# Performance work log

Hardware: AMD Instinct MI355X
Metric: run time of the kernel (lower is better)

Reference implementation:

```python
import jax, jax.numpy as jnp
import numpy as np

N_NODES = 100000
N_EDGES = 1600000
D_IN = 64
D_HID = 64
D_OUT = 10
N_GRAPHS = 512


def setup_inputs() -> dict:
    key = jax.random.key(0)
    ks = jax.random.split(key, 12)
    x = jax.random.normal(ks[0], (N_NODES, D_IN), dtype=jnp.float32)
    edge_index = jax.random.randint(ks[1], (2, N_EDGES), 0, N_NODES, dtype=jnp.int64)
    batch = jnp.sort(jax.random.randint(ks[2], (N_NODES,), 0, N_GRAPHS, dtype=jnp.int64))
    def lin_w(k, fan_in, fan_out):
        s = 1.0 / np.sqrt(fan_in)
        return jax.random.uniform(k, (fan_in, fan_out), jnp.float32, -s, s)
    # Per PyG GraphConv: lin_rel (with bias) on aggregated neighbors, lin_root (no bias) on self.
    params = {
        'W_rel1': lin_w(ks[3], D_IN, D_HID),  'b_rel1': jnp.zeros((D_HID,), jnp.float32), 'W_root1': lin_w(ks[4], D_IN, D_HID),
        'W_rel2': lin_w(ks[5], D_HID, D_HID), 'b_rel2': jnp.zeros((D_HID,), jnp.float32), 'W_root2': lin_w(ks[6], D_HID, D_HID),
        'W_rel3': lin_w(ks[7], D_HID, D_HID), 'b_rel3': jnp.zeros((D_HID,), jnp.float32), 'W_root3': lin_w(ks[8], D_HID, D_HID),
        'W_lin': lin_w(ks[9], D_HID, D_OUT),  'b_lin': jnp.zeros((D_OUT,), jnp.float32),
    }
    return {'x': x, 'edge_index': edge_index, 'batch': batch, **params}


def _graph_conv(x, src, dst, W_rel, b_rel, W_root):
    # sum-aggregate messages x[src] at dst nodes, then two linear maps
    agg = jax.ops.segment_sum(x[src], dst, num_segments=N_NODES)
    return agg @ W_rel + b_rel + x @ W_root


def reference(x, edge_index, batch,
              W_rel1, b_rel1, W_root1,
              W_rel2, b_rel2, W_root2,
              W_rel3, b_rel3, W_root3,
              W_lin, b_lin):
    src, dst = edge_index[0], edge_index[1]
    h = jax.nn.relu(_graph_conv(x, src, dst, W_rel1, b_rel1, W_root1))
    h = jax.nn.relu(_graph_conv(h, src, dst, W_rel2, b_rel2, W_root2))
    h = _graph_conv(h, src, dst, W_rel3, b_rel3, W_root3)
    # global_mean_pool over graph ids
    sums = jax.ops.segment_sum(h, batch, num_segments=N_GRAPHS)
    counts = jax.ops.segment_sum(jnp.ones((h.shape[0], 1), h.dtype), batch, num_segments=N_GRAPHS)
    pooled = sums / jnp.maximum(counts, 1.0)
    return pooled @ W_lin + b_lin
```

## Files before the change

kernel.cpp:

```cpp
#include <hip/hip_runtime.h>

#define NN 100000
#define NE 1600000
#define DF 64
#define NG 512
#define DOUT 10
#define NPART 8
#define PSZ 12500

typedef unsigned short u16;
typedef unsigned int   u32;
typedef __attribute__((ext_vector_type(8))) short short8;
typedef __attribute__((ext_vector_type(4))) float f32x4;

__device__ __forceinline__ float bflo(u32 u) { union { u32 u; float f; } x; x.u = u << 16;        return x.f; }
__device__ __forceinline__ float bfhi(u32 u) { union { u32 u; float f; } x; x.u = u & 0xFFFF0000u; return x.f; }
__device__ __forceinline__ u32 f2bf(float f) {
    union { float f; u32 u; } x; x.f = f;
    return (x.u + 0x7FFFu + ((x.u >> 16) & 1u)) >> 16;
}
__device__ __forceinline__ u32 pk(float lo, float hi) { return f2bf(lo) | (f2bf(hi) << 16); }

__global__ __launch_bounds__(256) void k_cursor_init(int* __restrict__ cursor) {
    int n = blockIdx.x * 256 + threadIdx.x;
    if (n < NN) cursor[n] = n << 6;
}

__global__ __launch_bounds__(256) void k_fill(const int* __restrict__ src,
                                              const int* __restrict__ dst,
                                              int* __restrict__ cursor,
                                              int* __restrict__ csr) {
    int part = blockIdx.x & (NPART - 1);
    int e = (blockIdx.x >> 3) * 256 + threadIdx.x;
    if (e >= NE) return;
    int d = __builtin_nontemporal_load(&dst[e]);
    if (d / PSZ != part) return;
    int pos = atomicAdd(&cursor[d], 1);
    if (pos < (d << 6) + 64) csr[pos] = __builtin_nontemporal_load(&src[e]);
}

__global__ __launch_bounds__(256) void k_cvt(const float* __restrict__ x,
                                             u16* __restrict__ xb) {
    int i = blockIdx.x * 256 + threadIdx.x;
    if (i >= NN * 8) return;
    const float4* p = (const float4*)x + (size_t)i * 2;
    float4 a = p[0], b = p[1];
    uint4 o;
    o.x = pk(a.x, a.y); o.y = pk(a.z, a.w);
    o.z = pk(b.x, b.y); o.w = pk(b.z, b.w);
    ((uint4*)xb)[i] = o;
}

__global__ __launch_bounds__(256) void k_wprep(const float* __restrict__ Wrel,
                                               const float* __restrict__ Wroot,
                                               u16* __restrict__ whi,
                                               u16* __restrict__ wlo) {
    int i = blockIdx.x * 256 + threadIdx.x;
    if (i >= 8192) return;
    int j  = i & 7;
    int l  = (i >> 3) & 63;
    int kh = (i >> 9) & 1;
    int ct = (i >> 10) & 3;
    int m  = i >> 12;
    int k = kh * 32 + ((l >> 4) << 3) + j;
    int o = ct * 16 + (l & 15);
    const float* W = m ? Wroot : Wrel;
    float v = W[k * 64 + o];
    u32 hi = f2bf(v);
    union { u32 u; float f; } hf; hf.u = hi << 16;
    u32 lo = f2bf(v - hf.f);
    whi[i] = (u16)hi;
    wlo[i] = (u16)lo;
}

template <bool RELU>
__global__ __launch_bounds__(256) void k_glin(const u16* __restrict__ hb,
                                              const int* __restrict__ csr,
                                              const int* __restrict__ cursor,
                                              const u16* __restrict__ whi,
                                              const u16* __restrict__ wlo,
                                              const float* __restrict__ brel,
                                              u16* __restrict__ outb) {
    __shared__ u16 sAgg[32][72];
    const int t = threadIdx.x;
    const int node0 = blockIdx.x * 32;

    {
        int n = node0 + (t >> 3);
        int c8 = (t & 7) << 3;
        int beg = n << 6;
        int cnt = cursor[n] - beg; if (cnt > 64) cnt = 64;
        const int* lst = csr + beg;
        float a0=0,a1=0,a2=0,a3=0,a4=0,a5=0,a6=0,a7=0;
        int j = 0;
        for (; j + 7 < cnt; j += 8) {
            int idx[8];
#pragma unroll
            for (int q = 0; q < 8; ++q) idx[q] = lst[j + q];
            uint4 v[8];
#pragma unroll
            for (int q = 0; q < 8; ++q) v[q] = *(const uint4*)(hb + (size_t)idx[q] * DF + c8);
#pragma unroll
            for (int q = 0; q < 8; ++q) {
                a0 += bflo(v[q].x); a1 += bfhi(v[q].x);
                a2 += bflo(v[q].y); a3 += bfhi(v[q].y);
                a4 += bflo(v[q].z); a5 += bfhi(v[q].z);
                a6 += bflo(v[q].w); a7 += bfhi(v[q].w);
            }
        }
        for (; j < cnt; ++j) {
            uint4 v = *(const uint4*)(hb + (size_t)lst[j] * DF + c8);
            a0 += bflo(v.x); a1 += bfhi(v.x);
            a2 += bflo(v.y); a3 += bfhi(v.y);
            a4 += bflo(v.z); a5 += bfhi(v.z);
            a6 += bflo(v.w); a7 += bfhi(v.w);
        }
        uint4 o;
        o.x = pk(a0,a1); o.y = pk(a2,a3); o.z = pk(a4,a5); o.w = pk(a6,a7);
        *(uint4*)&sAgg[t >> 3][c8] = o;
    }
    __syncthreads();

    const int w = t >> 6, l = t & 63;
    const int lh = l & 15, kg = l >> 4;
    const int ng = w >> 1;
    const int lnode = ng * 16 + lh;
    const int node = node0 + lnode;

    short8 bA0 = *(const short8*)&sAgg[lnode][kg * 8];
    short8 bA1 = *(const short8*)&sAgg[lnode][32 + kg * 8];
    const u16* ph = hb + (size_t)node * DF + kg * 8;
    short8 bH0 = *(const short8*)ph;
    short8 bH1 = *(const short8*)(ph + 32);

#pragma unroll
    for (int cc = 0; cc < 2; ++cc) {
        const int ct = (w & 1) * 2 + cc;
        const float4 bb = *(const float4*)(brel + ct * 16 + kg * 4);
        f32x4 acc = { bb.x, bb.y, bb.z, bb.w };
        const int lo8 = l * 8;
        short8 a0 = *(const short8*)(whi + ((0*4 + ct)*2 + 0)*512 + lo8);
        short8 a1 = *(const short8*)(whi + ((0*4 + ct)*2 + 1)*512 + lo8);
        short8 a2 = *(const short8*)(wlo + ((0*4 + ct)*2 + 0)*512 + lo8);
        short8 a3 = *(const short8*)(wlo + ((0*4 + ct)*2 + 1)*512 + lo8);
        short8 a4 = *(const short8*)(whi + ((1*4 + ct)*2 + 0)*512 + lo8);
        short8 a5 = *(const short8*)(whi + ((1*4 + ct)*2 + 1)*512 + lo8);
        short8 a6 = *(const short8*)(wlo + ((1*4 + ct)*2 + 0)*512 + lo8);
        short8 a7 = *(const short8*)(wlo + ((1*4 + ct)*2 + 1)*512 + lo8);
        acc = __builtin_amdgcn_mfma_f32_16x16x32_bf16(a0, bA0, acc, 0, 0, 0);
        acc = __builtin_amdgcn_mfma_f32_16x16x32_bf16(a1, bA1, acc, 0, 0, 0);
        acc = __builtin_amdgcn_mfma_f32_16x16x32_bf16(a2, bA0, acc, 0, 0, 0);
        acc = __builtin_amdgcn_mfma_f32_16x16x32_bf16(a3, bA1, acc, 0, 0, 0);
        acc = __builtin_amdgcn_mfma_f32_16x16x32_bf16(a4, bH0, acc, 0, 0, 0);
        acc = __builtin_amdgcn_mfma_f32_16x16x32_bf16(a5, bH1, acc, 0, 0, 0);
        acc = __builtin_amdgcn_mfma_f32_16x16x32_bf16(a6, bH0, acc, 0, 0, 0);
        acc = __builtin_amdgcn_mfma_f32_16x16x32_bf16(a7, bH1, acc, 0, 0, 0);
        if (RELU) {
            acc[0] = fmaxf(acc[0], 0.f); acc[1] = fmaxf(acc[1], 0.f);
            acc[2] = fmaxf(acc[2], 0.f); acc[3] = fmaxf(acc[3], 0.f);
        }
        uint2 o;
        o.x = pk(acc[0], acc[1]);
        o.y = pk(acc[2], acc[3]);
        *(uint2*)(outb + (size_t)node * DF + ct * 16 + kg * 4) = o;
    }
}

__global__ __launch_bounds__(256) void k_gstart(const int* __restrict__ batch,
                                                int* __restrict__ gstart) {
    int g = blockIdx.x * 256 + threadIdx.x;
    if (g > NG) return;
    int lo = 0, hi = NN;
    while (lo < hi) {
        int mid = (lo + hi) >> 1;
        if (batch[mid] < g) lo = mid + 1; else hi = mid;
    }
    gstart[g] = lo;
}

__global__ __launch_bounds__(256) void k_pool(const u16* __restrict__ hb,
                                              const int* __restrict__ gstart,
                                              float* __restrict__ pooled) {
    int g = blockIdx.x;
    int beg = gstart[g], end = gstart[g + 1];
    int lane = threadIdx.x & 63, wv = threadIdx.x >> 6;
    float acc = 0.f;
    for (int n = beg + wv; n < end; n += 4)
        acc += bflo((u32)hb[(size_t)n * DF + lane]);
    __shared__ float red[4][DF];
    red[wv][lane] = acc;
    __syncthreads();
    if (wv == 0) {
        float s = red[0][lane] + red[1][lane] + red[2][lane] + red[3][lane];
        pooled[(size_t)g * DF + lane] = s / fmaxf((float)(end - beg), 1.0f);
    }
}

__global__ __launch_bounds__(256) void k_head(const float* __restrict__ pooled,
                                              const float* __restrict__ Wlin,
                                              const float* __restrict__ blin,
                                              float* __restrict__ out) {
    int tid = blockIdx.x * 256 + threadIdx.x;
    if (tid >= NG * DOUT) return;
    int g = tid / DOUT;
    int j = tid - g * DOUT;
    float acc = blin[j];
#pragma unroll
    for (int k = 0; k < DF; ++k)
        acc += pooled[(size_t)g * DF + k] * Wlin[k * DOUT + j];
    out[(size_t)g * DOUT + j] = acc;
}

extern "C" void kernel_launch(void* const* d_in, const int* in_sizes, int n_in,
                              void* d_out, int out_size, void* d_ws, size_t ws_size,
                              hipStream_t stream) {
    (void)in_sizes; (void)n_in; (void)out_size; (void)ws_size;
    const float* x      = (const float*)d_in[0];
    const int*   edges  = (const int*)d_in[1];
    const int*   batch  = (const int*)d_in[2];
    const float* Wrel1  = (const float*)d_in[3];
    const float* brel1  = (const float*)d_in[4];
    const float* Wroot1 = (const float*)d_in[5];
    const float* Wrel2  = (const float*)d_in[6];
    const float* brel2  = (const float*)d_in[7];
    const float* Wroot2 = (const float*)d_in[8];
    const float* Wrel3  = (const float*)d_in[9];
    const float* brel3  = (const float*)d_in[10];
    const float* Wroot3 = (const float*)d_in[11];
    const float* Wlin   = (const float*)d_in[12];
    const float* blin   = (const float*)d_in[13];
    float* out = (float*)d_out;

    const int* src = edges;
    const int* dst = edges + NE;

    char* w = (char*)d_ws;
    u16* xb     = (u16*)(w);
    u16* hA     = (u16*)(w + 12800000);
    u16* hB     = (u16*)(w + 25600000);
    float* pooled = (float*)(w + 38400000);
    int* csr    = (int*)(w + 38531072);
    int* cursor = (int*)(w + 64131072);
    int* gstart = (int*)(w + 64531072);
    u16* whiB   = (u16*)(w + 64533504);
    u16* wloB   = (u16*)(w + 64533504 + 3*8192*2);

    dim3 blk(256);

    k_cursor_init<<<(NN + 255) / 256, blk, 0, stream>>>(cursor);
    k_fill<<<((NE + 255) / 256) * NPART, blk, 0, stream>>>(src, dst, cursor, csr);
    k_cvt<<<(NN * 8 + 255) / 256, blk, 0, stream>>>(x, xb);
    k_gstart<<<3, blk, 0, stream>>>(batch, gstart);
    k_wprep<<<32, blk, 0, stream>>>(Wrel1, Wroot1, whiB + 0*8192, wloB + 0*8192);
    k_wprep<<<32, blk, 0, stream>>>(Wrel2, Wroot2, whiB + 1*8192, wloB + 1*8192);
    k_wprep<<<32, blk, 0, stream>>>(Wrel3, Wroot3, whiB + 2*8192, wloB + 2*8192);

    dim3 gGL(NN / 32);

    k_glin<true><<<gGL, blk, 0, stream>>>(xb, csr, cursor, whiB + 0*8192, wloB + 0*8192, brel1, hA);
    k_glin<true><<<gGL, blk, 0, stream>>>(hA, csr, cursor, whiB + 1*8192, wloB + 1*8192, brel2, hB);
    k_glin<false><<<gGL, blk, 0, stream>>>(hB, csr, cursor, whiB + 2*8192, wloB + 2*8192, brel3, hA);

    k_pool<<<NG, blk, 0, stream>>>(hA, gstart, pooled);
    k_head<<<(NG * DOUT + 255) / 256, blk, 0, stream>>>(pooled, Wlin, blin, out);
}
```

Baseline: 338.3 us.

## Two-pass edge partitioning for CSR build and merge small prep kernels

```diff
diff --git a/kernel.cpp b/kernel.cpp
--- a/kernel.cpp
+++ b/kernel.cpp
@@ -7,9 +7,11 @@
 #define DOUT 10
 #define NPART 8
 #define PSZ 12500
+#define PCAP 220000
 
 typedef unsigned short u16;
 typedef unsigned int   u32;
+typedef unsigned long long u64;
 typedef __attribute__((ext_vector_type(8))) short short8;
 typedef __attribute__((ext_vector_type(4))) float f32x4;
 
@@ -21,22 +23,101 @@
 }
 __device__ __forceinline__ u32 pk(float lo, float hi) { return f2bf(lo) | (f2bf(hi) << 16); }
 
-__global__ __launch_bounds__(256) void k_cursor_init(int* __restrict__ cursor) {
-    int n = blockIdx.x * 256 + threadIdx.x;
-    if (n < NN) cursor[n] = n << 6;
-}
-
-__global__ __launch_bounds__(256) void k_fill(const int* __restrict__ src,
+__global__ __launch_bounds__(256) void k_prep(int* __restrict__ cursor,
+                                              int* __restrict__ pcur,
+                                              const int* __restrict__ batch,
+                                              int* __restrict__ gstart,
+                                              const float* __restrict__ Wr1,
+                                              const float* __restrict__ Wo1,
+                                              const float* __restrict__ Wr2,
+                                              const float* __restrict__ Wo2,
+                                              const float* __restrict__ Wr3,
+                                              const float* __restrict__ Wo3,
+                                              u16* __restrict__ whiB,
+                                              u16* __restrict__ wloB) {
+    const int b = blockIdx.x, t = threadIdx.x;
+    if (b < 392) {
+        int n = b * 256 + t;
+        if (n < NN) cursor[n] = n << 6;
+    } else if (b == 392) {
+        if (t < NPART) pcur[t] = 0;
+    } else if (b < 396) {
+        int g = (b - 393) * 256 + t;
+        if (g <= NG) {
+            int lo = 0, hi = NN;
+            while (lo < hi) {
+                int mid = (lo + hi) >> 1;
+                if (batch[mid] < g) lo = mid + 1; else hi = mid;
+            }
+            gstart[g] = lo;
+        }
+    } else {
+        int bb = b - 396;
+        int layer = bb >> 5;
+        int i = (bb & 31) * 256 + t;
+        int j  = i & 7;
+        int l  = (i >> 3) & 63;
+        int kh = (i >> 9) & 1;
+        int ct = (i >> 10) & 3;
+        int m  = i >> 12;
+        int k = kh * 32 + ((l >> 4) << 3) + j;
+        int o = ct * 16 + (l & 15);
+        const float* W;
+        if (layer == 0) W = m ? Wo1 : Wr1;
+        else if (layer == 1) W = m ? Wo2 : Wr2;
+        else W = m ? Wo3 : Wr3;
+        float v = W[k * 64 + o];
+        u32 hi = f2bf(v);
+        union { u32 u; float f; } hf; hf.u = hi << 16;
+        u32 lo = f2bf(v - hf.f);
+        whiB[layer * 8192 + i] = (u16)hi;
+        wloB[layer * 8192 + i] = (u16)lo;
+    }
+}
+
+__global__ __launch_bounds__(256) void k_part(const int* __restrict__ src,
                                               const int* __restrict__ dst,
-                                              int* __restrict__ cursor,
-                                              int* __restrict__ csr) {
-    int part = blockIdx.x & (NPART - 1);
-    int e = (blockIdx.x >> 3) * 256 + threadIdx.x;
-    if (e >= NE) return;
-    int d = __builtin_nontemporal_load(&dst[e]);
-    if (d / PSZ != part) return;
-    int pos = atomicAdd(&cursor[d], 1);
-    if (pos < (d << 6) + 64) csr[pos] = __builtin_nontemporal_load(&src[e]);
+                                              u64* __restrict__ pbuf,
+                                              int* __restrict__ pcur) {
+    __shared__ int lcnt[NPART];
+    __shared__ int lbase[NPART];
+    const int t = threadIdx.x;
+    if (t < NPART) lcnt[t] = 0;
+    __syncthreads();
+    int e = blockIdx.x * 256 + t;
+    int s = 0, d = 0, part = 0, loc = 0;
+    bool ok = (e < NE);
+    if (ok) {
+        d = __builtin_nontemporal_load(&dst[e]);
+        s = __builtin_nontemporal_load(&src[e]);
+        part = d / PSZ;
+        loc = atomicAdd(&lcnt[part], 1);
+    }
+    __syncthreads();
+    if (t < NPART) lbase[t] = atomicAdd(&pcur[t], lcnt[t]);
+    __syncthreads();
+    if (ok) {
+        int pos = lbase[part] + loc;
+        if (pos < PCAP)
+            pbuf[(size_t)part * PCAP + pos] = ((u64)(u32)d << 32) | (u32)s;
+    }
+}
+
+__global__ __launch_bounds__(256) void k_fill2(const u64* __restrict__ pbuf,
+                                               const int* __restrict__ pcur,
+                                               int* __restrict__ cursor,
+                                               int* __restrict__ csr) {
+    const int part = blockIdx.x & (NPART - 1);
+    const int bi = blockIdx.x >> 3;
+    const int nb = gridDim.x >> 3;
+    int cnt = pcur[part]; if (cnt > PCAP) cnt = PCAP;
+    const u64* lst = pbuf + (size_t)part * PCAP;
+    for (int i = bi * 256 + threadIdx.x; i < cnt; i += nb * 256) {
+        u64 p = __builtin_nontemporal_load(&lst[i]);
+        int d = (int)(p >> 32);
+        int pos = atomicAdd(&cursor[d], 1);
+        if (pos < (d << 6) + 64) csr[pos] = (int)(p & 0xFFFFFFFFu);
+    }
 }
 
 __global__ __launch_bounds__(256) void k_cvt(const float* __restrict__ x,
@@ -49,28 +130,6 @@
     o.x = pk(a.x, a.y); o.y = pk(a.z, a.w);
     o.z = pk(b.x, b.y); o.w = pk(b.z, b.w);
     ((uint4*)xb)[i] = o;
-}
-
-__global__ __launch_bounds__(256) void k_wprep(const float* __restrict__ Wrel,
-                                               const float* __restrict__ Wroot,
-                                               u16* __restrict__ whi,
-                                               u16* __restrict__ wlo) {
-    int i = blockIdx.x * 256 + threadIdx.x;
-    if (i >= 8192) return;
-    int j  = i & 7;
-    int l  = (i >> 3) & 63;
-    int kh = (i >> 9) & 1;
-    int ct = (i >> 10) & 3;
-    int m  = i >> 12;
-    int k = kh * 32 + ((l >> 4) << 3) + j;
-    int o = ct * 16 + (l & 15);
-    const float* W = m ? Wroot : Wrel;
-    float v = W[k * 64 + o];
-    u32 hi = f2bf(v);
-    union { u32 u; float f; } hf; hf.u = hi << 16;
-    u32 lo = f2bf(v - hf.f);
-    whi[i] = (u16)hi;
-    wlo[i] = (u16)lo;
 }
 
 template <bool RELU>
@@ -166,18 +225,6 @@
     }
 }
 
-__global__ __launch_bounds__(256) void k_gstart(const int* __restrict__ batch,
-                                                int* __restrict__ gstart) {
-    int g = blockIdx.x * 256 + threadIdx.x;
-    if (g > NG) return;
-    int lo = 0, hi = NN;
-    while (lo < hi) {
-        int mid = (lo + hi) >> 1;
-        if (batch[mid] < g) lo = mid + 1; else hi = mid;
-    }
-    gstart[g] = lo;
-}
-
 __global__ __launch_bounds__(256) void k_pool(const u16* __restrict__ hb,
                                               const int* __restrict__ gstart,
                                               float* __restrict__ pooled) {
@@ -235,25 +282,26 @@
     const int* dst = edges + NE;
 
     char* w = (char*)d_ws;
-    u16* xb     = (u16*)(w);
-    u16* hA     = (u16*)(w + 12800000);
-    u16* hB     = (u16*)(w + 25600000);
+    u16* xb       = (u16*)(w);
+    u16* hA       = (u16*)(w + 12800000);
+    u16* hB       = (u16*)(w + 25600000);
     float* pooled = (float*)(w + 38400000);
-    int* csr    = (int*)(w + 38531072);
-    int* cursor = (int*)(w + 64131072);
-    int* gstart = (int*)(w + 64531072);
-    u16* whiB   = (u16*)(w + 64533504);
-    u16* wloB   = (u16*)(w + 64533504 + 3*8192*2);
+    int* csr      = (int*)(w + 38531072);
+    int* cursor   = (int*)(w + 64131072);
+    int* gstart   = (int*)(w + 64531072);
+    u16* whiB     = (u16*)(w + 64533504);
+    u16* wloB     = (u16*)(w + 64582656);
+    u64* pbuf     = (u64*)(w + 64631808);
+    int* pcur     = (int*)(w + 78711808);
 
     dim3 blk(256);
 
-    k_cursor_init<<<(NN + 255) / 256, blk, 0, stream>>>(cursor);
-    k_fill<<<((NE + 255) / 256) * NPART, blk, 0, stream>>>(src, dst, cursor, csr);
+    k_prep<<<492, blk, 0, stream>>>(cursor, pcur, batch, gstart,
+                                    Wrel1, Wroot1, Wrel2, Wroot2, Wrel3, Wroot3,
+                                    whiB, wloB);
+    k_part<<<(NE + 255) / 256, blk, 0, stream>>>(src, dst, pbuf, pcur);
+    k_fill2<<<2048, blk, 0, stream>>>(pbuf, pcur, cursor, csr);
     k_cvt<<<(NN * 8 + 255) / 256, blk, 0, stream>>>(x, xb);
-    k_gstart<<<3, blk, 0, stream>>>(batch, gstart);
-    k_wprep<<<32, blk, 0, stream>>>(Wrel1, Wroot1, whiB + 0*8192, wloB + 0*8192);
-    k_wprep<<<32, blk, 0, stream>>>(Wrel2, Wroot2, whiB + 1*8192, wloB + 1*8192);
-    k_wprep<<<32, blk, 0, stream>>>(Wrel3, Wroot3, whiB + 2*8192, wloB + 2*8192);
 
     dim3 gGL(NN / 32);
 
```

New measurement: 398.2 us. 1.18x slower.
